# Performance work log

Hardware: AMD Instinct MI355X
Metric: run time of the kernel (lower is better)

Reference implementation:

```python
import jax, jax.numpy as jnp
import numpy as np

N_EMBD = 2048
N_HEAD = 16
N_KV_HEAD = 4
HEAD_DIM = N_EMBD // N_HEAD  # 128
N_REP = N_HEAD // N_KV_HEAD  # 4
ROPE_BASE = 1000000.0
B, T = 2, 2048


def _rotate_half(x):
    x1, x2 = jnp.split(x, 2, axis=-1)
    return jnp.concatenate([-x2, x1], axis=-1)


def _rope(q, k, t):
    # q: [b,t,h,d], k: [b,t,kvh,d]; full rotary (partial_rotary_factor=1.0)
    pos = jnp.arange(t, dtype=jnp.float32)
    inv_freq = 1.0 / (ROPE_BASE ** (jnp.arange(0, HEAD_DIM, 2, dtype=jnp.float32) / HEAD_DIM))
    ang = pos[:, None] * inv_freq[None, :]                      # [t, d/2]
    cos = jnp.concatenate([jnp.cos(ang), jnp.cos(ang)], -1)     # [t, d]
    sin = jnp.concatenate([jnp.sin(ang), jnp.sin(ang)], -1)
    cos = cos[None, :, None, :]
    sin = sin[None, :, None, :]
    q = q * cos + _rotate_half(q) * sin
    k = k * cos + _rotate_half(k) * sin
    return q, k


def setup_inputs() -> dict:
    key = jax.random.key(0)
    ks = jax.random.split(key, 9)
    std = 0.02
    proj_std = 0.02 / np.sqrt(2 * 24)
    return {
        "x": jax.random.normal(ks[0], (B, T, N_EMBD), dtype=jnp.float32),
        "Wq": jax.random.normal(ks[1], (N_EMBD, N_HEAD * HEAD_DIM), dtype=jnp.float32) * std,
        "bq": jnp.zeros((N_HEAD * HEAD_DIM,), dtype=jnp.float32),
        "Wk": jax.random.normal(ks[2], (N_EMBD, N_KV_HEAD * HEAD_DIM), dtype=jnp.float32) * std,
        "bk": jnp.zeros((N_KV_HEAD * HEAD_DIM,), dtype=jnp.float32),
        "Wv": jax.random.normal(ks[3], (N_EMBD, N_KV_HEAD * HEAD_DIM), dtype=jnp.float32) * std,
        "bv": jnp.zeros((N_KV_HEAD * HEAD_DIM,), dtype=jnp.float32),
        "Wo": jax.random.normal(ks[4], (N_EMBD, N_EMBD), dtype=jnp.float32) * proj_std,
        "bo": jnp.zeros((N_EMBD,), dtype=jnp.float32),
    }


def reference(x, Wq, bq, Wk, bk, Wv, bv, Wo, bo):
    b, t, _ = x.shape
    q = (x @ Wq + bq).reshape(b, t, N_HEAD, HEAD_DIM)
    k = (x @ Wk + bk).reshape(b, t, N_KV_HEAD, HEAD_DIM)
    v = (x @ Wv + bv).reshape(b, t, N_KV_HEAD, HEAD_DIM)
    q, k = _rope(q, k, t)
    # repeat_kv: expand kv heads by n_rep
    k = jnp.broadcast_to(k[:, :, :, None, :], (b, t, N_KV_HEAD, N_REP, HEAD_DIM)).reshape(b, t, N_HEAD, HEAD_DIM)
    v = jnp.broadcast_to(v[:, :, :, None, :], (b, t, N_KV_HEAD, N_REP, HEAD_DIM)).reshape(b, t, N_HEAD, HEAD_DIM)
    qh = q.transpose(0, 2, 1, 3)  # [b,h,t,d]
    kh = k.transpose(0, 2, 1, 3)
    vh = v.transpose(0, 2, 1, 3)
    causal = jnp.tril(jnp.ones((t, t), dtype=bool))[None, None]  # [1,1,t,t]
    bias = jnp.where(causal, 0.0, -1e9).astype(jnp.float32)
    scores = jnp.einsum('bhtd,bhTd->bhtT', qh, kh) / jnp.sqrt(jnp.float32(HEAD_DIM))
    attn_w = jax.nn.softmax(scores + bias, axis=-1)
    attn_out = jnp.einsum('bhtT,bhTd->bhtd', attn_w, vh)
    attn = attn_out.transpose(0, 2, 1, 3).reshape(b, t, N_EMBD)
    return attn @ Wo + bo
```

## Files before the change

kernel.cpp:

```cpp
#include <hip/hip_runtime.h>

typedef _Float16 f16x8 __attribute__((ext_vector_type(8)));
typedef _Float16 f16x4 __attribute__((ext_vector_type(4)));
typedef float    f32x4 __attribute__((ext_vector_type(4)));

__device__ __forceinline__ void gload16(const void* g, void* l) {
  __builtin_amdgcn_global_load_lds((const __attribute__((address_space(1))) void*)g,
                                   (__attribute__((address_space(3))) void*)l, 16, 0, 0);
}

__global__ __launch_bounds__(256) void cast_f32_f16(const float* __restrict__ src,
                                                    _Float16* __restrict__ dst, int n4) {
  int i = blockIdx.x * 256 + threadIdx.x;
  if (i < n4) {
    f32x4 v = *(const f32x4*)(src + (size_t)i * 4);
    f16x4 o;
    o[0] = (_Float16)v[0]; o[1] = (_Float16)v[1];
    o[2] = (_Float16)v[2]; o[3] = (_Float16)v[3];
    *(f16x4*)(dst + (size_t)i * 4) = o;
  }
}

__global__ __launch_bounds__(256) void wtrans_kernel(const float* __restrict__ src,
                                                     _Float16* __restrict__ dst,
                                                     int N, int K, int rowOff, int ldDst) {
  const int n0 = blockIdx.x * 64, k0 = blockIdx.y * 64;
  __shared__ float tile[64][65];
#pragma unroll
  for (int i = 0; i < 16; ++i) {
    int id = i * 256 + threadIdx.x;
    int kk = id >> 6, nn = id & 63;
    tile[kk][nn] = src[(size_t)(k0 + kk) * N + n0 + nn];
  }
  __syncthreads();
#pragma unroll
  for (int i = 0; i < 16; ++i) {
    int id = i * 256 + threadIdx.x;
    int nn = id >> 6, kk = id & 63;
    dst[(size_t)(rowOff + n0 + nn) * ldDst + k0 + kk] = (_Float16)tile[kk][nn];
  }
}

__global__ __launch_bounds__(256) void biaspack_kernel(const float* __restrict__ bq,
                                                       const float* __restrict__ bk,
                                                       const float* __restrict__ bv,
                                                       float* __restrict__ out) {
  int i = blockIdx.x * 256 + threadIdx.x;
  if (i < 3072) out[i] = (i < 2048) ? bq[i] : (i < 2560 ? bk[i - 2048] : bv[i - 2560]);
}

template <bool F16OUT>
__global__ __launch_bounds__(256) void gemm_nt(const _Float16* __restrict__ A,
                                               const _Float16* __restrict__ B,
                                               const float* __restrict__ bias,
                                               void* __restrict__ Cv,
                                               int M, int N, int K) {
  __shared__ __align__(16) _Float16 As[128][64];
  __shared__ __align__(16) _Float16 Bs[128][64];
  const int tid = threadIdx.x;
  const int lane = tid & 63, wave = tid >> 6;
  const int wr = wave >> 1, wc = wave & 1;
  const int r = lane & 15, g = lane >> 4;
  const int rb = blockIdx.y * 128, cb = blockIdx.x * 128;

  const int swz = ((tid & 7) ^ ((tid >> 3) & 7)) * 8;
  const _Float16* aSrc = A + (size_t)(rb + (tid >> 3)) * K + swz;
  const _Float16* bSrc = B + (size_t)(cb + (tid >> 3)) * K + swz;

  f32x4 acc[4][4] = {};

  for (int kt = 0; kt < K; kt += 64) {
    __syncthreads();
#pragma unroll
    for (int p = 0; p < 4; ++p) {
      gload16(aSrc + (size_t)(p * 32) * K + kt, (_Float16*)As + (p * 256 + wave * 64) * 8);
      gload16(bSrc + (size_t)(p * 32) * K + kt, (_Float16*)Bs + (p * 256 + wave * 64) * 8);
    }
    __syncthreads();
#pragma unroll
    for (int kk = 0; kk < 2; ++kk) {
      f16x8 af[4], bf[4];
#pragma unroll
      for (int m = 0; m < 4; ++m) {
        int row = wr * 64 + m * 16 + r;
        af[m] = *(const f16x8*)(&As[row][((kk * 4 + g) ^ (row & 7)) * 8]);
      }
#pragma unroll
      for (int n = 0; n < 4; ++n) {
        int row = wc * 64 + n * 16 + r;
        bf[n] = *(const f16x8*)(&Bs[row][((kk * 4 + g) ^ (row & 7)) * 8]);
      }
#pragma unroll
      for (int m = 0; m < 4; ++m)
#pragma unroll
        for (int n = 0; n < 4; ++n)
          acc[m][n] = __builtin_amdgcn_mfma_f32_16x16x32_f16(af[m], bf[n], acc[m][n], 0, 0, 0);
    }
  }

  float bvals[4];
#pragma unroll
  for (int n = 0; n < 4; ++n) bvals[n] = bias[cb + wc * 64 + n * 16 + r];
#pragma unroll
  for (int m = 0; m < 4; ++m) {
#pragma unroll
    for (int n = 0; n < 4; ++n) {
#pragma unroll
      for (int j = 0; j < 4; ++j) {
        int row = rb + wr * 64 + m * 16 + g * 4 + j;
        int col = cb + wc * 64 + n * 16 + r;
        float v = acc[m][n][j] + bvals[n];
        if (F16OUT)
          ((_Float16*)Cv)[(size_t)row * N + col] = (_Float16)v;
        else
          ((float*)Cv)[(size_t)row * N + col] = v;
      }
    }
  }
}

__global__ __launch_bounds__(256) void rope_kernel(_Float16* __restrict__ QKV) {
  const int tok = blockIdx.x;
  const int t = tok & 2047;
  __shared__ float cs[64], sn[64];
  if (threadIdx.x < 64) {
    int j = threadIdx.x;
    float freq = exp2f((float)(-2 * j) * (19.931568569324174f / 128.0f));
    float ang = (float)t * freq;
    cs[j] = cosf(ang);
    sn[j] = sinf(ang);
  }
  __syncthreads();
  _Float16* base = QKV + (size_t)tok * 3072;
  for (int idx = threadIdx.x; idx < 1280; idx += 256) {
    int head = idx >> 6, j = idx & 63;
    int cb = (head < 16) ? head * 128 : 2048 + (head - 16) * 128;
    _Float16* p = base + cb;
    float x1 = (float)p[j], x2 = (float)p[j + 64];
    float c = cs[j], s = sn[j];
    p[j]      = (_Float16)(x1 * c - x2 * s);
    p[j + 64] = (_Float16)(x2 * c + x1 * s);
  }
}

__global__ __launch_bounds__(256) void vtrans_kernel(const _Float16* __restrict__ QKV,
                                                     _Float16* __restrict__ Vt) {
  const int bk = blockIdx.z;
  const int t0 = blockIdx.x * 64, d0 = blockIdx.y * 64;
  const int b = bk >> 2, kvh = bk & 3;
  __shared__ _Float16 tile[64][65];
  const _Float16* src = QKV + (size_t)b * 2048 * 3072 + 2560 + kvh * 128;
#pragma unroll
  for (int i = 0; i < 16; ++i) {
    int id = i * 256 + threadIdx.x;
    int tt = id >> 6, dd = id & 63;
    tile[tt][dd] = src[(size_t)(t0 + tt) * 3072 + d0 + dd];
  }
  __syncthreads();
  _Float16* dst = Vt + (size_t)bk * 128 * 2048;
#pragma unroll
  for (int i = 0; i < 16; ++i) {
    int id = i * 256 + threadIdx.x;
    int dd = id >> 6, tt = id & 63;
    dst[(size_t)(d0 + dd) * 2048 + t0 + tt] = tile[tt][dd];
  }
}

__global__ __launch_bounds__(512) void attn_kernel(const _Float16* __restrict__ QKV,
                                                   const _Float16* __restrict__ Vt,
                                                   _Float16* __restrict__ O) {
  const int bid = blockIdx.x;
  const int b = bid >> 8;
  const int ii = bid & 255;
  const int h = ii >> 4;
  const int qtr = ii & 15;
  const int qt = b ? 15 - qtr : qtr;
  const int tid = threadIdx.x;
  const int wave = tid >> 6, lane = tid & 63;
  const int r = lane & 15, g = lane >> 4;
  const int q0 = qt * 128 + wave * 16;
  const int kvh = h >> 2;
  const _Float16* Qb  = QKV + (size_t)b * 2048 * 3072 + h * 128;
  const _Float16* Kb  = QKV + (size_t)b * 2048 * 3072 + 2048 + kvh * 128;
  const _Float16* Vtg = Vt + (size_t)(b * 4 + kvh) * 128 * 2048;

  __shared__ __align__(16) _Float16 Klds[64][128];
  __shared__ __align__(16) _Float16 Vlds[128][64];
  __shared__ __align__(16) _Float16 Plds[8][16][64];

  const _Float16* kSrc = Kb  + (size_t)(tid >> 4) * 3072 + (((tid & 15) ^ ((tid >> 4) & 7)) * 8);
  const _Float16* vSrc = Vtg + (size_t)(tid >> 3) * 2048 + (((tid & 7) ^ ((tid >> 3) & 7)) * 8);

  f16x8 qf[4];
  {
    const float qsc = 0.08838834764831845f * 1.4426950408889634f;
    const _Float16* qrow = Qb + (size_t)(q0 + r) * 3072 + g * 8;
#pragma unroll
    for (int c = 0; c < 4; ++c) {
      f16x8 v = *(const f16x8*)(qrow + c * 32);
#pragma unroll
      for (int i = 0; i < 8; ++i) v[i] = (_Float16)((float)v[i] * qsc);
      qf[c] = v;
    }
  }

  f32x4 oacc[8] = {};
  float mrun = -1e30f, lrun = 0.f;
  const int kend = qt * 128 + 128;
  const int qlim = q0 + 16;

  for (int kb = 0; kb < kend; kb += 64) {
    gload16(kSrc + (size_t)kb * 3072,        (_Float16*)Klds + (wave * 64) * 8);
    gload16(kSrc + (size_t)(kb + 32) * 3072, (_Float16*)Klds + (512 + wave * 64) * 8);
    gload16(vSrc + kb,                       (_Float16*)Vlds + (wave * 64) * 8);
    gload16(vSrc + (size_t)64 * 2048 + kb,   (_Float16*)Vlds + (512 + wave * 64) * 8);
    __syncthreads();
    if (kb < qlim) {
      f32x4 sT[4] = {};
#pragma unroll
      for (int c = 0; c < 4; ++c) {
#pragma unroll
        for (int n = 0; n < 4; ++n) {
          f16x8 kf = *(const f16x8*)(&Klds[n * 16 + r][(((c * 4 + g) ^ (r & 7)) * 8)]);
          sT[n] = __builtin_amdgcn_mfma_f32_16x16x32_f16(kf, qf[c], sT[n], 0, 0, 0);
        }
      }
      if (kb + 63 > q0) {
#pragma unroll
        for (int n = 0; n < 4; ++n)
#pragma unroll
          for (int j = 0; j < 4; ++j) {
            int kg = kb + n * 16 + g * 4 + j;
            if (kg > q0 + r) sT[n][j] = -1e30f;
          }
      }
      float mt = -1e30f;
#pragma unroll
      for (int n = 0; n < 4; ++n)
#pragma unroll
        for (int j = 0; j < 4; ++j) mt = fmaxf(mt, sT[n][j]);
      mt = fmaxf(mt, __shfl_xor(mt, 16));
      mt = fmaxf(mt, __shfl_xor(mt, 32));
      if (__any(mt > mrun)) {
        float mnew = fmaxf(mrun, mt);
        float alpha = exp2f(mrun - mnew);
        lrun *= alpha;
        float al[4];
#pragma unroll
        for (int jj = 0; jj < 4; ++jj) al[jj] = __shfl(alpha, g * 4 + jj);
#pragma unroll
        for (int dt = 0; dt < 8; ++dt)
#pragma unroll
          for (int jj = 0; jj < 4; ++jj) oacc[dt][jj] *= al[jj];
        mrun = mnew;
      }
      float p[4][4];
      float rs = 0.f;
#pragma unroll
      for (int n = 0; n < 4; ++n)
#pragma unroll
        for (int j = 0; j < 4; ++j) {
          p[n][j] = exp2f(sT[n][j] - mrun);
          rs += p[n][j];
        }
      rs += __shfl_xor(rs, 16);
      rs += __shfl_xor(rs, 32);
      lrun += rs;
      asm volatile("" ::: "memory");
#pragma unroll
      for (int n = 0; n < 4; ++n) {
        f16x4 p4;
#pragma unroll
        for (int j = 0; j < 4; ++j) p4[j] = (_Float16)p[n][j];
        int c16s = (2 * n + (g >> 1)) ^ (r & 7);
        *(f16x4*)(&Plds[wave][r][c16s * 8 + (g & 1) * 4]) = p4;
      }
      asm volatile("s_waitcnt lgkmcnt(0)" ::: "memory");
      __builtin_amdgcn_sched_barrier(0);
      f16x8 pa0 = *(const f16x8*)(&Plds[wave][r][((g) ^ (r & 7)) * 8]);
      f16x8 pa1 = *(const f16x8*)(&Plds[wave][r][((4 + g) ^ (r & 7)) * 8]);
#pragma unroll
      for (int dt = 0; dt < 8; ++dt) {
        f16x8 vf0 = *(const f16x8*)(&Vlds[dt * 16 + r][((g) ^ (r & 7)) * 8]);
        oacc[dt] = __builtin_amdgcn_mfma_f32_16x16x32_f16(pa0, vf0, oacc[dt], 0, 0, 0);
        f16x8 vf1 = *(const f16x8*)(&Vlds[dt * 16 + r][((4 + g) ^ (r & 7)) * 8]);
        oacc[dt] = __builtin_amdgcn_mfma_f32_16x16x32_f16(pa1, vf1, oacc[dt], 0, 0, 0);
      }
    }
    __syncthreads();
  }

  float linv = 1.0f / lrun;
  float li[4];
#pragma unroll
  for (int jj = 0; jj < 4; ++jj) li[jj] = __shfl(linv, g * 4 + jj);
#pragma unroll
  for (int dt = 0; dt < 8; ++dt)
#pragma unroll
    for (int jj = 0; jj < 4; ++jj)
      O[(size_t)(b * 2048 + q0 + g * 4 + jj) * 2048 + h * 128 + dt * 16 + r] =
          (_Float16)(oacc[dt][jj] * li[jj]);
}

extern "C" void kernel_launch(void* const* d_in, const int* in_sizes, int n_in,
                              void* d_out, int out_size, void* d_ws, size_t ws_size,
                              hipStream_t stream) {
  const float* x  = (const float*)d_in[0];
  const float* Wq = (const float*)d_in[1];
  const float* bq = (const float*)d_in[2];
  const float* Wk = (const float*)d_in[3];
  const float* bk = (const float*)d_in[4];
  const float* Wv = (const float*)d_in[5];
  const float* bv = (const float*)d_in[6];
  const float* Wo = (const float*)d_in[7];
  const float* bo = (const float*)d_in[8];
  float* out = (float*)d_out;

  char* ws = (char*)d_ws;
  constexpr size_t QKV_OFF  = 0;
  constexpr size_t VT_OFF   = 25165824;
  constexpr size_t ATTN_OFF = VT_OFF + 4194304;
  constexpr size_t WT_OFF   = ATTN_OFF + 16777216;
  constexpr size_t BIAS_OFF = WT_OFF + 12582912;
  _Float16* QKV  = (_Float16*)(ws + QKV_OFF);
  _Float16* Vt   = (_Float16*)(ws + VT_OFF);
  _Float16* attn = (_Float16*)(ws + ATTN_OFF);
  _Float16* WT   = (_Float16*)(ws + WT_OFF);
  float*    bqkv = (float*)(ws + BIAS_OFF);
  _Float16* xb = (_Float16*)d_out;

  cast_f32_f16<<<8192, 256, 0, stream>>>(x, xb, (2 * 2048 * 2048) / 4);
  wtrans_kernel<<<dim3(32, 32), 256, 0, stream>>>(Wq, WT, 2048, 2048, 0, 2048);
  wtrans_kernel<<<dim3(8, 32), 256, 0, stream>>>(Wk, WT, 512, 2048, 2048, 2048);
  wtrans_kernel<<<dim3(8, 32), 256, 0, stream>>>(Wv, WT, 512, 2048, 2560, 2048);
  biaspack_kernel<<<12, 256, 0, stream>>>(bq, bk, bv, bqkv);
  gemm_nt<true><<<dim3(3072 / 128, 4096 / 128), 256, 0, stream>>>(xb, WT, bqkv, QKV, 4096, 3072, 2048);
  wtrans_kernel<<<dim3(32, 32), 256, 0, stream>>>(Wo, WT, 2048, 2048, 0, 2048);
  rope_kernel<<<4096, 256, 0, stream>>>(QKV);
  vtrans_kernel<<<dim3(32, 2, 8), 256, 0, stream>>>(QKV, Vt);
  attn_kernel<<<512, 512, 0, stream>>>(QKV, Vt, attn);
  gemm_nt<false><<<dim3(2048 / 128, 4096 / 128), 256, 0, stream>>>(attn, WT, bo, out, 4096, 2048, 2048);
}
```

Before: 225.6 us.

## Double-buffer K/V tiles in attention, fuse QKV weight transposes, vectorize RoPE

The attention kernel now keeps two LDS buffers for K and V. It prefetches the next tile with global_load_lds while computing on the current one, using explicit vmcnt waits and s_barrier, and raises wave priority around the MFMA loops. The three Q/K/V weight-transpose launches are merged into one kernel, and RoPE now uses 8-wide f16 vector loads and stores. The extra buffering doubles K/V LDS use, which may reduce occupancy of the 512-thread attention blocks.

```diff
diff --git a/kernel.cpp b/kernel.cpp
--- a/kernel.cpp
+++ b/kernel.cpp
@@ -18,6 +18,31 @@
     o[0] = (_Float16)v[0]; o[1] = (_Float16)v[1];
     o[2] = (_Float16)v[2]; o[3] = (_Float16)v[3];
     *(f16x4*)(dst + (size_t)i * 4) = o;
+  }
+}
+
+__global__ __launch_bounds__(256) void wqkvtrans_kernel(const float* __restrict__ Wq,
+                                                        const float* __restrict__ Wk,
+                                                        const float* __restrict__ Wv,
+                                                        _Float16* __restrict__ dst) {
+  const int n0 = blockIdx.x * 64, k0 = blockIdx.y * 64;
+  const float* src; int N, nb;
+  if (n0 < 2048)      { src = Wq; N = 2048; nb = n0; }
+  else if (n0 < 2560) { src = Wk; N = 512;  nb = n0 - 2048; }
+  else                { src = Wv; N = 512;  nb = n0 - 2560; }
+  __shared__ float tile[64][65];
+#pragma unroll
+  for (int i = 0; i < 16; ++i) {
+    int id = i * 256 + threadIdx.x;
+    int kk = id >> 6, nn = id & 63;
+    tile[kk][nn] = src[(size_t)(k0 + kk) * N + nb + nn];
+  }
+  __syncthreads();
+#pragma unroll
+  for (int i = 0; i < 16; ++i) {
+    int id = i * 256 + threadIdx.x;
+    int nn = id >> 6, kk = id & 63;
+    dst[(size_t)(n0 + nn) * 2048 + k0 + kk] = (_Float16)tile[kk][nn];
   }
 }
 
@@ -132,14 +157,23 @@
   }
   __syncthreads();
   _Float16* base = QKV + (size_t)tok * 3072;
-  for (int idx = threadIdx.x; idx < 1280; idx += 256) {
-    int head = idx >> 6, j = idx & 63;
+  int idx = threadIdx.x;
+  if (idx < 160) {
+    int head = idx >> 3, j0 = (idx & 7) * 8;
     int cb = (head < 16) ? head * 128 : 2048 + (head - 16) * 128;
     _Float16* p = base + cb;
-    float x1 = (float)p[j], x2 = (float)p[j + 64];
-    float c = cs[j], s = sn[j];
-    p[j]      = (_Float16)(x1 * c - x2 * s);
-    p[j + 64] = (_Float16)(x2 * c + x1 * s);
+    f16x8 a = *(const f16x8*)(p + j0);
+    f16x8 b2 = *(const f16x8*)(p + 64 + j0);
+    f16x8 oa, ob;
+#pragma unroll
+    for (int e = 0; e < 8; ++e) {
+      float c = cs[j0 + e], s = sn[j0 + e];
+      float x1 = (float)a[e], x2 = (float)b2[e];
+      oa[e] = (_Float16)(x1 * c - x2 * s);
+      ob[e] = (_Float16)(x2 * c + x1 * s);
+    }
+    *(f16x8*)(p + j0) = oa;
+    *(f16x8*)(p + 64 + j0) = ob;
   }
 }
 
@@ -184,8 +218,8 @@
   const _Float16* Kb  = QKV + (size_t)b * 2048 * 3072 + 2048 + kvh * 128;
   const _Float16* Vtg = Vt + (size_t)(b * 4 + kvh) * 128 * 2048;
 
-  __shared__ __align__(16) _Float16 Klds[64][128];
-  __shared__ __align__(16) _Float16 Vlds[128][64];
+  __shared__ __align__(16) _Float16 Klds[2][64][128];
+  __shared__ __align__(16) _Float16 Vlds[2][128][64];
   __shared__ __align__(16) _Float16 Plds[8][16][64];
 
   const _Float16* kSrc = Kb  + (size_t)(tid >> 4) * 3072 + (((tid & 15) ^ ((tid >> 4) & 7)) * 8);
@@ -203,28 +237,46 @@
       qf[c] = v;
     }
   }
+  asm volatile("s_waitcnt vmcnt(0)" ::: "memory");
 
   f32x4 oacc[8] = {};
   float mrun = -1e30f, lrun = 0.f;
   const int kend = qt * 128 + 128;
   const int qlim = q0 + 16;
 
+  {
+    gload16(kSrc,                          &Klds[0][0][0] + (wave * 64) * 8);
+    gload16(kSrc + (size_t)32 * 3072,      &Klds[0][0][0] + (512 + wave * 64) * 8);
+    gload16(vSrc,                          &Vlds[0][0][0] + (wave * 64) * 8);
+    gload16(vSrc + (size_t)64 * 2048,      &Vlds[0][0][0] + (512 + wave * 64) * 8);
+  }
+
+  int cur = 0;
   for (int kb = 0; kb < kend; kb += 64) {
-    gload16(kSrc + (size_t)kb * 3072,        (_Float16*)Klds + (wave * 64) * 8);
-    gload16(kSrc + (size_t)(kb + 32) * 3072, (_Float16*)Klds + (512 + wave * 64) * 8);
-    gload16(vSrc + kb,                       (_Float16*)Vlds + (wave * 64) * 8);
-    gload16(vSrc + (size_t)64 * 2048 + kb,   (_Float16*)Vlds + (512 + wave * 64) * 8);
-    __syncthreads();
+    if (kb + 64 < kend) {
+      int nb = kb + 64, nxt = cur ^ 1;
+      gload16(kSrc + (size_t)nb * 3072,        &Klds[nxt][0][0] + (wave * 64) * 8);
+      gload16(kSrc + (size_t)(nb + 32) * 3072, &Klds[nxt][0][0] + (512 + wave * 64) * 8);
+      gload16(vSrc + nb,                       &Vlds[nxt][0][0] + (wave * 64) * 8);
+      gload16(vSrc + (size_t)64 * 2048 + nb,   &Vlds[nxt][0][0] + (512 + wave * 64) * 8);
+      asm volatile("s_waitcnt vmcnt(4)" ::: "memory");
+    } else {
+      asm volatile("s_waitcnt vmcnt(0)" ::: "memory");
+    }
+    __builtin_amdgcn_s_barrier();
+    __builtin_amdgcn_sched_barrier(0);
     if (kb < qlim) {
       f32x4 sT[4] = {};
+      __builtin_amdgcn_s_setprio(1);
 #pragma unroll
       for (int c = 0; c < 4; ++c) {
 #pragma unroll
         for (int n = 0; n < 4; ++n) {
-          f16x8 kf = *(const f16x8*)(&Klds[n * 16 + r][(((c * 4 + g) ^ (r & 7)) * 8)]);
+          f16x8 kf = *(const f16x8*)(&Klds[cur][n * 16 + r][(((c * 4 + g) ^ (r & 7)) * 8)]);
           sT[n] = __builtin_amdgcn_mfma_f32_16x16x32_f16(kf, qf[c], sT[n], 0, 0, 0);
         }
       }
+      __builtin_amdgcn_s_setprio(0);
       if (kb + 63 > q0) {
 #pragma unroll
         for (int n = 0; n < 4; ++n)
@@ -279,15 +331,20 @@
       __builtin_amdgcn_sched_barrier(0);
       f16x8 pa0 = *(const f16x8*)(&Plds[wave][r][((g) ^ (r & 7)) * 8]);
       f16x8 pa1 = *(const f16x8*)(&Plds[wave][r][((4 + g) ^ (r & 7)) * 8]);
+      __builtin_amdgcn_s_setprio(1);
 #pragma unroll
       for (int dt = 0; dt < 8; ++dt) {
-        f16x8 vf0 = *(const f16x8*)(&Vlds[dt * 16 + r][((g) ^ (r & 7)) * 8]);
+        f16x8 vf0 = *(const f16x8*)(&Vlds[cur][dt * 16 + r][((g) ^ (r & 7)) * 8]);
         oacc[dt] = __builtin_amdgcn_mfma_f32_16x16x32_f16(pa0, vf0, oacc[dt], 0, 0, 0);
-        f16x8 vf1 = *(const f16x8*)(&Vlds[dt * 16 + r][((4 + g) ^ (r & 7)) * 8]);
+        f16x8 vf1 = *(const f16x8*)(&Vlds[cur][dt * 16 + r][((4 + g) ^ (r & 7)) * 8]);
         oacc[dt] = __builtin_amdgcn_mfma_f32_16x16x32_f16(pa1, vf1, oacc[dt], 0, 0, 0);
       }
-    }
-    __syncthreads();
+      __builtin_amdgcn_s_setprio(0);
+    }
+    __builtin_amdgcn_sched_barrier(0);
+    __builtin_amdgcn_s_barrier();
+    __builtin_amdgcn_sched_barrier(0);
+    cur ^= 1;
   }
 
   float linv = 1.0f / lrun;
@@ -330,9 +387,7 @@
   _Float16* xb = (_Float16*)d_out;
 
   cast_f32_f16<<<8192, 256, 0, stream>>>(x, xb, (2 * 2048 * 2048) / 4);
-  wtrans_kernel<<<dim3(32, 32), 256, 0, stream>>>(Wq, WT, 2048, 2048, 0, 2048);
-  wtrans_kernel<<<dim3(8, 32), 256, 0, stream>>>(Wk, WT, 512, 2048, 2048, 2048);
-  wtrans_kernel<<<dim3(8, 32), 256, 0, stream>>>(Wv, WT, 512, 2048, 2560, 2048);
+  wqkvtrans_kernel<<<dim3(48, 32), 256, 0, stream>>>(Wq, Wk, Wv, WT);
   biaspack_kernel<<<12, 256, 0, stream>>>(bq, bk, bv, bqkv);
   gemm_nt<true><<<dim3(3072 / 128, 4096 / 128), 256, 0, stream>>>(xb, WT, bqkv, QKV, 4096, 3072, 2048);
   wtrans_kernel<<<dim3(32, 32), 256, 0, stream>>>(Wo, WT, 2048, 2048, 0, 2048);
```

New measurement: 216.6 us. 4.0% less time.
